# Kernel tuning notes

Hardware: AMD Instinct MI355X
Metric: run time of the kernel (lower is better)

## Reference

```python
import math
import jax, jax.numpy as jnp
import numpy as np

B, N, D, L = 8, 4096, 512, 64


def setup_inputs() -> dict:
    key = jax.random.key(0)
    ks = jax.random.split(key, 8)
    feats = jax.random.normal(ks[0], (B, N, D), dtype=jnp.float32)
    coords = jax.random.uniform(ks[1], (B, N, 2), dtype=jnp.float32)
    mask = jax.random.bernoulli(ks[2], 0.5, (B, N))  # True = padding (excluded)
    z = jax.random.normal(ks[3], (L, D), dtype=jnp.float32) * 0.02
    # xavier_uniform with gain=0.05 for square DxD weights: bound = gain*sqrt(6/(2D))
    bound = 0.05 * math.sqrt(6.0 / (2 * D))
    Wq = jax.random.uniform(ks[4], (D, D), minval=-bound, maxval=bound, dtype=jnp.float32)
    Wk = jax.random.uniform(ks[5], (D, D), minval=-bound, maxval=bound, dtype=jnp.float32)
    Wv = jax.random.uniform(ks[6], (D, D), minval=-bound, maxval=bound, dtype=jnp.float32)
    Wo = jax.random.uniform(ks[7], (D, D), minval=-bound, maxval=bound, dtype=jnp.float32)
    bo = jnp.zeros((D,), dtype=jnp.float32)
    return {"feats": feats, "coords": coords, "mask": mask, "z": z,
            "Wq": Wq, "Wk": Wk, "Wv": Wv, "Wo": Wo, "bo": bo}


def reference(feats, coords, mask, z, Wq, Wk, Wv, Wo, bo):
    Bb, Nn, Dd = feats.shape
    Ll = z.shape[0]
    temp = math.sqrt(Dd)
    q_all = z @ Wq.T  # [L, D] — one query per learned token

    def per_sample(f, m):
        nvalid = jnp.sum(~m)
        # stable sort: valid tokens (mask=False) first, original order preserved
        order = jnp.argsort(m.astype(jnp.int32), stable=True)
        sf = f[order]  # [N, D], first nvalid rows are the valid feats
        mu = sf.mean(-1, keepdims=True)
        var = sf.var(-1, keepdims=True)
        ln = (sf - mu) / jnp.sqrt(var + 1e-5)
        # segment assignment: seg_size = max(1, nvalid // L); token i -> segment i//seg_size
        seg_size = jnp.maximum(1, nvalid // Ll)
        pos = jnp.arange(Nn)
        seg = pos // seg_size
        tok_valid = (pos < nvalid) & (seg < Ll)  # tokens past L*seg_size are dropped (matches torch)
        seg_id = jnp.where(tok_valid, seg, Ll)  # dummy segment L for excluded tokens
        K = ln @ Wk.T  # [N, D]
        V = ln @ Wv.T  # [N, D]
        logits = jnp.clip(jnp.sum(q_all[jnp.minimum(seg, Ll - 1)] * K, -1) / temp, -5.0, 5.0)
        m_seg = jax.ops.segment_max(jnp.where(tok_valid, logits, -jnp.inf), seg_id, num_segments=Ll + 1)
        m_safe = jnp.where(jnp.isfinite(m_seg), m_seg, 0.0)
        e = jnp.where(tok_valid, jnp.exp(logits - m_safe[seg_id]), 0.0)
        denom = jax.ops.segment_sum(e, seg_id, num_segments=Ll + 1)[:Ll]            # [L]
        num = jax.ops.segment_sum(e[:, None] * V, seg_id, num_segments=Ll + 1)[:Ll]  # [L, D]
        nonempty = denom > 0
        Zattn = jnp.where(nonempty[:, None], num / jnp.maximum(denom, 1e-30)[:, None], z)
        out = Zattn @ Wo.T + bo
        return jnp.where(nvalid == 0, z, out)

    return jax.vmap(per_sample)(feats, mask)
```

## Files before the change

kernel.cpp:

```cpp
#include <hip/hip_runtime.h>
#include <math.h>

#define Bn 8
#define Nn 4096
#define Dn 512
#define Ln 64

template<int TN, bool BT, int NPART, bool SCALE>
__device__ __forceinline__ void gemm_tile(
    const float* __restrict__ A, size_t apstride, int m0,
    const float* __restrict__ B, int n0, int kbase, int ksteps,
    const float* __restrict__ sv,
    float* __restrict__ dst,
    float (*As)[68], float (*Bs)[132], int tid)
{
    const int ty = tid >> 4;
    const int tx = tid & 15;
    float acc[4][TN / 16];
    #pragma unroll
    for (int m = 0; m < 4; m++)
        #pragma unroll
        for (int n = 0; n < TN / 16; n++) acc[m][n] = 0.f;

    for (int s = 0; s < ksteps; s++) {
        const int k0 = kbase + s * 16;
        {
            int r = tid >> 2, kq = tid & 3;
            float4 v = *(const float4*)&A[(size_t)(m0 + r) * Dn + k0 + kq * 4];
            #pragma unroll
            for (int p = 1; p < NPART; p++) {
                float4 w = *(const float4*)&A[(size_t)p * apstride +
                                              (size_t)(m0 + r) * Dn + k0 + kq * 4];
                v.x += w.x; v.y += w.y; v.z += w.z; v.w += w.w;
            }
            if (SCALE) { float sc = sv[r]; v.x *= sc; v.y *= sc; v.z *= sc; v.w *= sc; }
            As[kq * 4 + 0][r] = v.x;
            As[kq * 4 + 1][r] = v.y;
            As[kq * 4 + 2][r] = v.z;
            As[kq * 4 + 3][r] = v.w;
        }
        #pragma unroll
        for (int rep = 0; rep < TN / 64; rep++) {
            int lin = tid + rep * 256;
            if (!BT) {
                int kk = lin / (TN / 4), jq = lin % (TN / 4);
                *(float4*)&Bs[kk][jq * 4] =
                    *(const float4*)&B[(size_t)(k0 + kk) * Dn + n0 + jq * 4];
            } else {
                int j = lin >> 2, kq = lin & 3;
                float4 v = *(const float4*)&B[(size_t)(n0 + j) * Dn + k0 + kq * 4];
                Bs[kq * 4 + 0][j] = v.x;
                Bs[kq * 4 + 1][j] = v.y;
                Bs[kq * 4 + 2][j] = v.z;
                Bs[kq * 4 + 3][j] = v.w;
            }
        }
        __syncthreads();
        #pragma unroll
        for (int kk = 0; kk < 16; kk++) {
            float4 a = *(const float4*)&As[kk][ty * 4];
            float av[4] = {a.x, a.y, a.z, a.w};
            if (TN == 64) {
                float4 b = *(const float4*)&Bs[kk][tx * 4];
                float bv[4] = {b.x, b.y, b.z, b.w};
                #pragma unroll
                for (int m = 0; m < 4; m++)
                    #pragma unroll
                    for (int n = 0; n < 4; n++) acc[m][n] += av[m] * bv[n];
            } else {
                float4 b0 = *(const float4*)&Bs[kk][tx * 8];
                float4 b1 = *(const float4*)&Bs[kk][tx * 8 + 4];
                float bv[8] = {b0.x, b0.y, b0.z, b0.w, b1.x, b1.y, b1.z, b1.w};
                #pragma unroll
                for (int m = 0; m < 4; m++)
                    #pragma unroll
                    for (int n = 0; n < 8; n++) acc[m][n % (TN/16)] += av[m] * bv[n];
            }
        }
        __syncthreads();
    }
    #pragma unroll
    for (int m = 0; m < 4; m++) {
        size_t base = (size_t)(m0 + ty * 4 + m) * Dn + n0;
        if (TN == 64) {
            float4 o = {acc[m][0], acc[m][1], acc[m][2], acc[m][3]};
            *(float4*)&dst[base + tx * 4] = o;
        } else {
            float4 o0 = {acc[m][0], acc[m][1], acc[m][2], acc[m][3]};
            float4 o1 = {acc[m][4], acc[m][5], acc[m][6], acc[m][7]};
            *(float4*)&dst[base + tx * 8] = o0;
            *(float4*)&dst[base + tx * 8 + 4] = o1;
        }
    }
}

__global__ void __launch_bounds__(256) kA_prep(
    const float* __restrict__ Wo, const float* __restrict__ Wv,
    const float* __restrict__ z,  const float* __restrict__ Wq,
    const unsigned char* __restrict__ maskbytes,
    float* __restrict__ wp, float* __restrict__ qp, float* __restrict__ wozp,
    int* __restrict__ nvalid, int* __restrict__ idx)
{
    __shared__ float As[16][68];
    __shared__ float Bs[16][132];
    __shared__ int scanbuf[256];
    __shared__ int cflags[4];

    int tid = threadIdx.x;
    int gb = blockIdx.x;

    if (gb < 256) {
        int ks = gb & 7;  int t = gb >> 3;
        int rt = t >> 2, ct = t & 3;
        gemm_tile<128, false, 1, false>(Wo, 0, rt * 64, Wv, ct * 128,
                                        ks * 64, 4, nullptr,
                                        wp + (size_t)ks * 262144, As, Bs, tid);
        return;
    }
    if (gb < 288) {
        int t = gb - 256; int ks = t & 3; int nt = t >> 2;
        gemm_tile<64, true, 1, false>(z, 0, 0, Wq, nt * 64,
                                      ks * 128, 8, nullptr,
                                      qp + (size_t)ks * 32768, As, Bs, tid);
        return;
    }
    if (gb < 320) {
        int t = gb - 288; int ks = t & 3; int nt = t >> 2;
        gemm_tile<64, true, 1, false>(z, 0, 0, Wo, nt * 64,
                                      ks * 128, 8, nullptr,
                                      wozp + (size_t)ks * 32768, As, Bs, tid);
        return;
    }

    int b = gb - 320;
    if (tid == 0) { cflags[0] = 0; cflags[1] = 0; cflags[2] = 0; }
    __syncthreads();
    int lge2 = 0, lb1 = 0, lm = 0;
    for (int p = tid; p < 4096; p += 256) {
        unsigned int v = maskbytes[p];
        if (v > 1u) lge2 = 1;
        if (v != 0u) {
            if ((p & 3) == 1) lb1 = 1;
            if ((p & 3) != 0) lm = 1;
        }
    }
    if (lge2) atomicOr(&cflags[0], 1);
    if (lb1)  atomicOr(&cflags[1], 1);
    if (lm)   atomicOr(&cflags[2], 1);
    __syncthreads();
    if (tid == 0) cflags[3] = cflags[0] ? (cflags[1] ? 2 : 4) : (cflags[2] ? 1 : 4);
    __syncthreads();
    int w = cflags[3];

    int base = tid * 16;
    int cnt = 0;
    int validbits[16];
    for (int e = 0; e < 16; e++) {
        int i = base + e;
        size_t byteoff = ((size_t)b * Nn + i) * (size_t)w;
        unsigned int nz = 0;
        for (int q = 0; q < w; q++) nz |= maskbytes[byteoff + q];
        int valid = (nz == 0) ? 1 : 0;
        validbits[e] = valid;
        cnt += valid;
    }
    scanbuf[tid] = cnt;
    __syncthreads();
    for (int off = 1; off < 256; off <<= 1) {
        int v = (tid >= off) ? scanbuf[tid - off] : 0;
        __syncthreads();
        scanbuf[tid] += v;
        __syncthreads();
    }
    int pos = scanbuf[tid] - cnt;
    for (int e = 0; e < 16; e++) {
        if (validbits[e]) { idx[b * Nn + pos] = base + e; pos++; }
    }
    if (tid == 255) nvalid[b] = scanbuf[255];
}

__global__ void __launch_bounds__(256) kB_qk(
    const float* __restrict__ qp, const float* __restrict__ Wk,
    const float* __restrict__ wp,
    float* __restrict__ qkp, float* __restrict__ wov)
{
    __shared__ float As[16][68];
    __shared__ float Bs[16][132];
    int tid = threadIdx.x;
    int gb = blockIdx.x;
    if (gb < 64) {
        int ks = gb & 7; int nt = gb >> 3;
        gemm_tile<64, false, 4, false>(qp, 32768, 0, Wk, nt * 64,
                                       ks * 64, 4, nullptr,
                                       qkp + (size_t)ks * 32768, As, Bs, tid);
        return;
    }
    int lin = (gb - 64) * 256 + tid;
    float4 v = {0.f, 0.f, 0.f, 0.f};
    #pragma unroll
    for (int p = 0; p < 8; p++) {
        float4 w = *(const float4*)&wp[(size_t)p * 262144 + (size_t)lin * 4];
        v.x += w.x; v.y += w.y; v.z += w.z; v.w += w.w;
    }
    *(float4*)&wov[(size_t)lin * 4] = v;
}

__global__ void __launch_bounds__(256) kE_tokens(
    const float* __restrict__ feats, const int* __restrict__ idx,
    const int* __restrict__ nvalid, const float* __restrict__ qkp,
    float* __restrict__ s_out, float* __restrict__ den_out)
{
    __shared__ float sred[4 * Dn];
    __shared__ float dred[4];
    int tid = threadIdx.x;
    int wv = tid >> 6;
    int lane = tid & 63;
    int b = blockIdx.x / Ln;
    int l = blockIdx.x % Ln;
    int nv = nvalid[b];
    int seg_size = nv / Ln; if (seg_size < 1) seg_size = 1;
    int used = Ln * seg_size; if (used > nv) used = nv;
    int r0 = l * seg_size;
    int r1 = r0 + seg_size; if (r1 > used) r1 = used;

    float4 qa = {0.f,0.f,0.f,0.f}, qb = {0.f,0.f,0.f,0.f};
    #pragma unroll
    for (int p = 0; p < 8; p++) {
        const float4* q4 = (const float4*)(qkp + (size_t)p * 32768 +
                                           (size_t)l * Dn + lane * 8);
        float4 a = q4[0], c = q4[1];
        qa.x += a.x; qa.y += a.y; qa.z += a.z; qa.w += a.w;
        qb.x += c.x; qb.y += c.y; qb.z += c.z; qb.w += c.w;
    }
    float qf[8] = {qa.x, qa.y, qa.z, qa.w, qb.x, qb.y, qb.z, qb.w};

    float sacc[8] = {0,0,0,0,0,0,0,0};
    float dacc = 0.f;
    const float inv_d = 1.0f / (float)Dn;
    const float inv_temp = 1.0f / 22.62741699796952f;

    for (int r = r0 + wv * 2; r < r1; r += 8) {
        int has2 = (r + 1 < r1);
        int t0 = idx[b * Nn + r];
        int t1 = has2 ? idx[b * Nn + r + 1] : t0;
        const float4* p0 = (const float4*)(feats + ((size_t)b * Nn + t0) * Dn + lane * 8);
        const float4* p1 = (const float4*)(feats + ((size_t)b * Nn + t1) * Dn + lane * 8);
        float4 xa0 = p0[0], xb0 = p0[1];
        float4 xa1 = p1[0], xb1 = p1[1];
        float x0[8] = {xa0.x, xa0.y, xa0.z, xa0.w, xb0.x, xb0.y, xb0.z, xb0.w};
        float x1[8] = {xa1.x, xa1.y, xa1.z, xa1.w, xb1.x, xb1.y, xb1.z, xb1.w};
        float sum0 = 0.f, ssq0 = 0.f, sum1 = 0.f, ssq1 = 0.f;
        #pragma unroll
        for (int j = 0; j < 8; j++) {
            sum0 += x0[j]; ssq0 += x0[j] * x0[j];
            sum1 += x1[j]; ssq1 += x1[j] * x1[j];
        }
        #pragma unroll
        for (int off = 32; off > 0; off >>= 1) {
            sum0 += __shfl_xor(sum0, off);
            ssq0 += __shfl_xor(ssq0, off);
            sum1 += __shfl_xor(sum1, off);
            ssq1 += __shfl_xor(ssq1, off);
        }
        float mu0 = sum0 * inv_d, mu1 = sum1 * inv_d;
        float rstd0 = rsqrtf(ssq0 * inv_d - mu0 * mu0 + 1e-5f);
        float rstd1 = rsqrtf(ssq1 * inv_d - mu1 * mu1 + 1e-5f);
        float ln0[8], ln1[8];
        float dot0 = 0.f, dot1 = 0.f;
        #pragma unroll
        for (int j = 0; j < 8; j++) {
            ln0[j] = (x0[j] - mu0) * rstd0; dot0 += ln0[j] * qf[j];
            ln1[j] = (x1[j] - mu1) * rstd1; dot1 += ln1[j] * qf[j];
        }
        #pragma unroll
        for (int off = 32; off > 0; off >>= 1) {
            dot0 += __shfl_xor(dot0, off);
            dot1 += __shfl_xor(dot1, off);
        }
        float lg0 = fminf(5.0f, fmaxf(-5.0f, dot0 * inv_temp));
        float lg1 = fminf(5.0f, fmaxf(-5.0f, dot1 * inv_temp));
        float e0 = expf(lg0);
        float e1 = has2 ? expf(lg1) : 0.f;
        #pragma unroll
        for (int j = 0; j < 8; j++) sacc[j] += e0 * ln0[j] + e1 * ln1[j];
        dacc += e0 + e1;
    }

    #pragma unroll
    for (int j = 0; j < 8; j++) sred[wv * Dn + lane * 8 + j] = sacc[j];
    if (lane == 0) dred[wv] = dacc;
    __syncthreads();
    for (int e = tid; e < Dn; e += 256) {
        float v = sred[e] + sred[Dn + e] + sred[2 * Dn + e] + sred[3 * Dn + e];
        s_out[(size_t)blockIdx.x * Dn + e] = v;
    }
    if (tid == 0) den_out[blockIdx.x] = dred[0] + dred[1] + dred[2] + dred[3];
}

__global__ void __launch_bounds__(256) kG_gemm(
    const float* __restrict__ s, const float* __restrict__ den,
    const float* __restrict__ wov, float* __restrict__ op)
{
    __shared__ float As[16][68];
    __shared__ float Bs[16][132];
    __shared__ float ssv[64];
    int tid = threadIdx.x;
    int gb = blockIdx.x;
    int ks = gb & 7; int t = gb >> 3;
    int rt = t >> 2, ct = t & 3;
    int m0 = rt * 64;
    if (tid < 64) {
        float dv = den[m0 + tid];
        ssv[tid] = (dv > 0.f) ? 1.f / dv : 0.f;
    }
    __syncthreads();
    gemm_tile<128, true, 1, true>(s, 0, m0, wov, ct * 128,
                                  ks * 64, 4, ssv,
                                  op + (size_t)ks * 262144, As, Bs, tid);
}

__global__ void __launch_bounds__(256) kH_epilogue(
    const float* __restrict__ op, const float* __restrict__ den,
    const int* __restrict__ nvalid, const float* __restrict__ wozp,
    const float* __restrict__ z, const float* __restrict__ bo,
    float* __restrict__ out)
{
    int lin = blockIdx.x * 256 + threadIdx.x;
    int row = lin >> 7;
    int col = (lin & 127) * 4;
    int b = row >> 6, l = row & 63;
    float4 v;
    if (nvalid[b] == 0) {
        v = *(const float4*)&z[(size_t)l * Dn + col];
    } else {
        float4 bv = *(const float4*)&bo[col];
        float dv = den[row];
        if (dv > 0.f) {
            float4 a = {0.f, 0.f, 0.f, 0.f};
            #pragma unroll
            for (int p = 0; p < 8; p++) {
                float4 w = *(const float4*)&op[(size_t)p * 262144 + (size_t)row * Dn + col];
                a.x += w.x; a.y += w.y; a.z += w.z; a.w += w.w;
            }
            v.x = a.x + bv.x; v.y = a.y + bv.y; v.z = a.z + bv.z; v.w = a.w + bv.w;
        } else {
            float4 a = {0.f, 0.f, 0.f, 0.f};
            #pragma unroll
            for (int p = 0; p < 4; p++) {
                float4 w = *(const float4*)&wozp[(size_t)p * 32768 + (size_t)l * Dn + col];
                a.x += w.x; a.y += w.y; a.z += w.z; a.w += w.w;
            }
            v.x = a.x + bv.x; v.y = a.y + bv.y; v.z = a.z + bv.z; v.w = a.w + bv.w;
        }
    }
    *(float4*)&out[(size_t)row * Dn + col] = v;
}

extern "C" void kernel_launch(void* const* d_in, const int* in_sizes, int n_in,
                              void* d_out, int out_size, void* d_ws, size_t ws_size,
                              hipStream_t stream) {
    const float* feats = (const float*)d_in[0];
    const unsigned char* maskb = (const unsigned char*)d_in[2];
    const float* z  = (const float*)d_in[3];
    const float* Wq = (const float*)d_in[4];
    const float* Wk = (const float*)d_in[5];
    const float* Wv = (const float*)d_in[6];
    const float* Wo = (const float*)d_in[7];
    const float* bo = (const float*)d_in[8];
    float* out = (float*)d_out;

    int*   nvalid = (int*)d_ws;
    int*   idx    = nvalid + 64;
    float* fbase  = (float*)(idx + Bn * Nn);
    float* qp     = fbase;
    float* wozp   = qp   + 4 * 32768;
    float* qkp    = wozp + 4 * 32768;
    float* wov    = qkp  + 8 * 32768;
    float* sbuf   = wov  + 262144;
    float* den    = sbuf + 262144;
    float* wp     = den  + 1024;
    float* op     = wp;

    kA_prep<<<328, 256, 0, stream>>>(Wo, Wv, z, Wq, maskb, wp, qp, wozp, nvalid, idx);
    kB_qk<<<320, 256, 0, stream>>>(qp, Wk, wp, qkp, wov);
    kE_tokens<<<Bn * Ln, 256, 0, stream>>>(feats, idx, nvalid, qkp, sbuf, den);
    kG_gemm<<<256, 256, 0, stream>>>(sbuf, den, wov, op);
    kH_epilogue<<<256, 256, 0, stream>>>(op, den, nvalid, wozp, z, bo, out);
}
```

Baseline: 148.9 us.

## Fuse five kernels into one cooperative kernel with grid-wide syncs

Merges the prep, QK/Wov reduction, token, GEMM and epilogue kernels into a single cooperative launch of 512 blocks, with grid.sync() between phases. The aim is to remove four kernel launch boundaries and their drain and ramp gaps. In exchange every phase runs on a fixed 512-block grid, so some phases leave blocks idle. Shared memory per block rises to the union of all phases, and grid syncs add their own cost. Residency of 512 blocks must be guaranteed for the cooperative launch to succeed.

```diff
diff --git a/kernel.cpp b/kernel.cpp
--- a/kernel.cpp
+++ b/kernel.cpp
@@ -1,5 +1,8 @@
 #include <hip/hip_runtime.h>
+#include <hip/hip_cooperative_groups.h>
 #include <math.h>
+
+namespace cg = cooperative_groups;
 
 #define Bn 8
 #define Nn 4096
@@ -8,10 +11,10 @@
 
 template<int TN, bool BT, int NPART, bool SCALE>
 __device__ __forceinline__ void gemm_tile(
-    const float* __restrict__ A, size_t apstride, int m0,
-    const float* __restrict__ B, int n0, int kbase, int ksteps,
-    const float* __restrict__ sv,
-    float* __restrict__ dst,
+    const float* A, size_t apstride, int m0,
+    const float* B, int n0, int kbase, int ksteps,
+    const float* sv,
+    float* dst,
     float (*As)[68], float (*Bs)[132], int tid)
 {
     const int ty = tid >> 4;
@@ -94,17 +97,24 @@
     }
 }
 
-__global__ void __launch_bounds__(256) kA_prep(
-    const float* __restrict__ Wo, const float* __restrict__ Wv,
-    const float* __restrict__ z,  const float* __restrict__ Wq,
-    const unsigned char* __restrict__ maskbytes,
-    float* __restrict__ wp, float* __restrict__ qp, float* __restrict__ wozp,
-    int* __restrict__ nvalid, int* __restrict__ idx)
+__global__ void __launch_bounds__(256) k_fused(
+    const float* __restrict__ feats, const unsigned char* __restrict__ maskbytes,
+    const float* __restrict__ z, const float* __restrict__ Wq,
+    const float* __restrict__ Wk, const float* __restrict__ Wv,
+    const float* __restrict__ Wo, const float* __restrict__ bo,
+    float* __restrict__ out,
+    int* nvalid, int* idx, float* qp, float* wozp, float* qkp,
+    float* wov, float* sbuf, float* den, float* wp)
 {
+    cg::grid_group grid = cg::this_grid();
+
     __shared__ float As[16][68];
     __shared__ float Bs[16][132];
     __shared__ int scanbuf[256];
     __shared__ int cflags[4];
+    __shared__ float sred[4 * Dn];
+    __shared__ float dred[4];
+    __shared__ float ssv[64];
 
     int tid = threadIdx.x;
     int gb = blockIdx.x;
@@ -115,245 +125,219 @@
         gemm_tile<128, false, 1, false>(Wo, 0, rt * 64, Wv, ct * 128,
                                         ks * 64, 4, nullptr,
                                         wp + (size_t)ks * 262144, As, Bs, tid);
-        return;
-    }
-    if (gb < 288) {
+    } else if (gb < 288) {
         int t = gb - 256; int ks = t & 3; int nt = t >> 2;
         gemm_tile<64, true, 1, false>(z, 0, 0, Wq, nt * 64,
                                       ks * 128, 8, nullptr,
                                       qp + (size_t)ks * 32768, As, Bs, tid);
-        return;
-    }
-    if (gb < 320) {
+    } else if (gb < 320) {
         int t = gb - 288; int ks = t & 3; int nt = t >> 2;
         gemm_tile<64, true, 1, false>(z, 0, 0, Wo, nt * 64,
                                       ks * 128, 8, nullptr,
                                       wozp + (size_t)ks * 32768, As, Bs, tid);
-        return;
-    }
-
-    int b = gb - 320;
-    if (tid == 0) { cflags[0] = 0; cflags[1] = 0; cflags[2] = 0; }
-    __syncthreads();
-    int lge2 = 0, lb1 = 0, lm = 0;
-    for (int p = tid; p < 4096; p += 256) {
-        unsigned int v = maskbytes[p];
-        if (v > 1u) lge2 = 1;
-        if (v != 0u) {
-            if ((p & 3) == 1) lb1 = 1;
-            if ((p & 3) != 0) lm = 1;
-        }
-    }
-    if (lge2) atomicOr(&cflags[0], 1);
-    if (lb1)  atomicOr(&cflags[1], 1);
-    if (lm)   atomicOr(&cflags[2], 1);
-    __syncthreads();
-    if (tid == 0) cflags[3] = cflags[0] ? (cflags[1] ? 2 : 4) : (cflags[2] ? 1 : 4);
-    __syncthreads();
-    int w = cflags[3];
-
-    int base = tid * 16;
-    int cnt = 0;
-    int validbits[16];
-    for (int e = 0; e < 16; e++) {
-        int i = base + e;
-        size_t byteoff = ((size_t)b * Nn + i) * (size_t)w;
-        unsigned int nz = 0;
-        for (int q = 0; q < w; q++) nz |= maskbytes[byteoff + q];
-        int valid = (nz == 0) ? 1 : 0;
-        validbits[e] = valid;
-        cnt += valid;
-    }
-    scanbuf[tid] = cnt;
-    __syncthreads();
-    for (int off = 1; off < 256; off <<= 1) {
-        int v = (tid >= off) ? scanbuf[tid - off] : 0;
-        __syncthreads();
-        scanbuf[tid] += v;
-        __syncthreads();
-    }
-    int pos = scanbuf[tid] - cnt;
-    for (int e = 0; e < 16; e++) {
-        if (validbits[e]) { idx[b * Nn + pos] = base + e; pos++; }
-    }
-    if (tid == 255) nvalid[b] = scanbuf[255];
-}
-
-__global__ void __launch_bounds__(256) kB_qk(
-    const float* __restrict__ qp, const float* __restrict__ Wk,
-    const float* __restrict__ wp,
-    float* __restrict__ qkp, float* __restrict__ wov)
-{
-    __shared__ float As[16][68];
-    __shared__ float Bs[16][132];
-    int tid = threadIdx.x;
-    int gb = blockIdx.x;
+    } else if (gb < 328) {
+        int b = gb - 320;
+        if (tid == 0) { cflags[0] = 0; cflags[1] = 0; cflags[2] = 0; }
+        __syncthreads();
+        int lge2 = 0, lb1 = 0, lm = 0;
+        for (int p = tid; p < 4096; p += 256) {
+            unsigned int v = maskbytes[p];
+            if (v > 1u) lge2 = 1;
+            if (v != 0u) {
+                if ((p & 3) == 1) lb1 = 1;
+                if ((p & 3) != 0) lm = 1;
+            }
+        }
+        if (lge2) atomicOr(&cflags[0], 1);
+        if (lb1)  atomicOr(&cflags[1], 1);
+        if (lm)   atomicOr(&cflags[2], 1);
+        __syncthreads();
+        if (tid == 0) cflags[3] = cflags[0] ? (cflags[1] ? 2 : 4) : (cflags[2] ? 1 : 4);
+        __syncthreads();
+        int w = cflags[3];
+
+        int base = tid * 16;
+        int cnt = 0;
+        int validbits[16];
+        for (int e = 0; e < 16; e++) {
+            int i = base + e;
+            size_t byteoff = ((size_t)b * Nn + i) * (size_t)w;
+            unsigned int nz = 0;
+            for (int q = 0; q < w; q++) nz |= maskbytes[byteoff + q];
+            int valid = (nz == 0) ? 1 : 0;
+            validbits[e] = valid;
+            cnt += valid;
+        }
+        scanbuf[tid] = cnt;
+        __syncthreads();
+        for (int off = 1; off < 256; off <<= 1) {
+            int v = (tid >= off) ? scanbuf[tid - off] : 0;
+            __syncthreads();
+            scanbuf[tid] += v;
+            __syncthreads();
+        }
+        int pos = scanbuf[tid] - cnt;
+        for (int e = 0; e < 16; e++) {
+            if (validbits[e]) { idx[b * Nn + pos] = base + e; pos++; }
+        }
+        if (tid == 255) nvalid[b] = scanbuf[255];
+    }
+    __threadfence();
+    grid.sync();
+
     if (gb < 64) {
         int ks = gb & 7; int nt = gb >> 3;
         gemm_tile<64, false, 4, false>(qp, 32768, 0, Wk, nt * 64,
                                        ks * 64, 4, nullptr,
                                        qkp + (size_t)ks * 32768, As, Bs, tid);
-        return;
-    }
-    int lin = (gb - 64) * 256 + tid;
-    float4 v = {0.f, 0.f, 0.f, 0.f};
-    #pragma unroll
-    for (int p = 0; p < 8; p++) {
-        float4 w = *(const float4*)&wp[(size_t)p * 262144 + (size_t)lin * 4];
-        v.x += w.x; v.y += w.y; v.z += w.z; v.w += w.w;
-    }
-    *(float4*)&wov[(size_t)lin * 4] = v;
-}
-
-__global__ void __launch_bounds__(256) kE_tokens(
-    const float* __restrict__ feats, const int* __restrict__ idx,
-    const int* __restrict__ nvalid, const float* __restrict__ qkp,
-    float* __restrict__ s_out, float* __restrict__ den_out)
-{
-    __shared__ float sred[4 * Dn];
-    __shared__ float dred[4];
-    int tid = threadIdx.x;
-    int wv = tid >> 6;
-    int lane = tid & 63;
-    int b = blockIdx.x / Ln;
-    int l = blockIdx.x % Ln;
-    int nv = nvalid[b];
-    int seg_size = nv / Ln; if (seg_size < 1) seg_size = 1;
-    int used = Ln * seg_size; if (used > nv) used = nv;
-    int r0 = l * seg_size;
-    int r1 = r0 + seg_size; if (r1 > used) r1 = used;
-
-    float4 qa = {0.f,0.f,0.f,0.f}, qb = {0.f,0.f,0.f,0.f};
-    #pragma unroll
-    for (int p = 0; p < 8; p++) {
-        const float4* q4 = (const float4*)(qkp + (size_t)p * 32768 +
-                                           (size_t)l * Dn + lane * 8);
-        float4 a = q4[0], c = q4[1];
-        qa.x += a.x; qa.y += a.y; qa.z += a.z; qa.w += a.w;
-        qb.x += c.x; qb.y += c.y; qb.z += c.z; qb.w += c.w;
-    }
-    float qf[8] = {qa.x, qa.y, qa.z, qa.w, qb.x, qb.y, qb.z, qb.w};
-
-    float sacc[8] = {0,0,0,0,0,0,0,0};
-    float dacc = 0.f;
-    const float inv_d = 1.0f / (float)Dn;
-    const float inv_temp = 1.0f / 22.62741699796952f;
-
-    for (int r = r0 + wv * 2; r < r1; r += 8) {
-        int has2 = (r + 1 < r1);
-        int t0 = idx[b * Nn + r];
-        int t1 = has2 ? idx[b * Nn + r + 1] : t0;
-        const float4* p0 = (const float4*)(feats + ((size_t)b * Nn + t0) * Dn + lane * 8);
-        const float4* p1 = (const float4*)(feats + ((size_t)b * Nn + t1) * Dn + lane * 8);
-        float4 xa0 = p0[0], xb0 = p0[1];
-        float4 xa1 = p1[0], xb1 = p1[1];
-        float x0[8] = {xa0.x, xa0.y, xa0.z, xa0.w, xb0.x, xb0.y, xb0.z, xb0.w};
-        float x1[8] = {xa1.x, xa1.y, xa1.z, xa1.w, xb1.x, xb1.y, xb1.z, xb1.w};
-        float sum0 = 0.f, ssq0 = 0.f, sum1 = 0.f, ssq1 = 0.f;
-        #pragma unroll
-        for (int j = 0; j < 8; j++) {
-            sum0 += x0[j]; ssq0 += x0[j] * x0[j];
-            sum1 += x1[j]; ssq1 += x1[j] * x1[j];
-        }
-        #pragma unroll
-        for (int off = 32; off > 0; off >>= 1) {
-            sum0 += __shfl_xor(sum0, off);
-            ssq0 += __shfl_xor(ssq0, off);
-            sum1 += __shfl_xor(sum1, off);
-            ssq1 += __shfl_xor(ssq1, off);
-        }
-        float mu0 = sum0 * inv_d, mu1 = sum1 * inv_d;
-        float rstd0 = rsqrtf(ssq0 * inv_d - mu0 * mu0 + 1e-5f);
-        float rstd1 = rsqrtf(ssq1 * inv_d - mu1 * mu1 + 1e-5f);
-        float ln0[8], ln1[8];
-        float dot0 = 0.f, dot1 = 0.f;
-        #pragma unroll
-        for (int j = 0; j < 8; j++) {
-            ln0[j] = (x0[j] - mu0) * rstd0; dot0 += ln0[j] * qf[j];
-            ln1[j] = (x1[j] - mu1) * rstd1; dot1 += ln1[j] * qf[j];
-        }
-        #pragma unroll
-        for (int off = 32; off > 0; off >>= 1) {
-            dot0 += __shfl_xor(dot0, off);
-            dot1 += __shfl_xor(dot1, off);
-        }
-        float lg0 = fminf(5.0f, fmaxf(-5.0f, dot0 * inv_temp));
-        float lg1 = fminf(5.0f, fmaxf(-5.0f, dot1 * inv_temp));
-        float e0 = expf(lg0);
-        float e1 = has2 ? expf(lg1) : 0.f;
-        #pragma unroll
-        for (int j = 0; j < 8; j++) sacc[j] += e0 * ln0[j] + e1 * ln1[j];
-        dacc += e0 + e1;
-    }
-
-    #pragma unroll
-    for (int j = 0; j < 8; j++) sred[wv * Dn + lane * 8 + j] = sacc[j];
-    if (lane == 0) dred[wv] = dacc;
-    __syncthreads();
-    for (int e = tid; e < Dn; e += 256) {
-        float v = sred[e] + sred[Dn + e] + sred[2 * Dn + e] + sred[3 * Dn + e];
-        s_out[(size_t)blockIdx.x * Dn + e] = v;
-    }
-    if (tid == 0) den_out[blockIdx.x] = dred[0] + dred[1] + dred[2] + dred[3];
-}
-
-__global__ void __launch_bounds__(256) kG_gemm(
-    const float* __restrict__ s, const float* __restrict__ den,
-    const float* __restrict__ wov, float* __restrict__ op)
-{
-    __shared__ float As[16][68];
-    __shared__ float Bs[16][132];
-    __shared__ float ssv[64];
-    int tid = threadIdx.x;
-    int gb = blockIdx.x;
-    int ks = gb & 7; int t = gb >> 3;
-    int rt = t >> 2, ct = t & 3;
-    int m0 = rt * 64;
-    if (tid < 64) {
-        float dv = den[m0 + tid];
-        ssv[tid] = (dv > 0.f) ? 1.f / dv : 0.f;
-    }
-    __syncthreads();
-    gemm_tile<128, true, 1, true>(s, 0, m0, wov, ct * 128,
-                                  ks * 64, 4, ssv,
-                                  op + (size_t)ks * 262144, As, Bs, tid);
-}
-
-__global__ void __launch_bounds__(256) kH_epilogue(
-    const float* __restrict__ op, const float* __restrict__ den,
-    const int* __restrict__ nvalid, const float* __restrict__ wozp,
-    const float* __restrict__ z, const float* __restrict__ bo,
-    float* __restrict__ out)
-{
-    int lin = blockIdx.x * 256 + threadIdx.x;
-    int row = lin >> 7;
-    int col = (lin & 127) * 4;
-    int b = row >> 6, l = row & 63;
-    float4 v;
-    if (nvalid[b] == 0) {
-        v = *(const float4*)&z[(size_t)l * Dn + col];
-    } else {
-        float4 bv = *(const float4*)&bo[col];
-        float dv = den[row];
-        if (dv > 0.f) {
-            float4 a = {0.f, 0.f, 0.f, 0.f};
-            #pragma unroll
-            for (int p = 0; p < 8; p++) {
-                float4 w = *(const float4*)&op[(size_t)p * 262144 + (size_t)row * Dn + col];
-                a.x += w.x; a.y += w.y; a.z += w.z; a.w += w.w;
-            }
-            v.x = a.x + bv.x; v.y = a.y + bv.y; v.z = a.z + bv.z; v.w = a.w + bv.w;
+    } else if (gb < 320) {
+        int lin = (gb - 64) * 256 + tid;
+        float4 v = {0.f, 0.f, 0.f, 0.f};
+        #pragma unroll
+        for (int p = 0; p < 8; p++) {
+            float4 w = *(const float4*)&wp[(size_t)p * 262144 + (size_t)lin * 4];
+            v.x += w.x; v.y += w.y; v.z += w.z; v.w += w.w;
+        }
+        *(float4*)&wov[(size_t)lin * 4] = v;
+    }
+    __threadfence();
+    grid.sync();
+
+    {
+        int wv = tid >> 6;
+        int lane = tid & 63;
+        int b = gb / Ln;
+        int l = gb % Ln;
+        int nv = nvalid[b];
+        int seg_size = nv / Ln; if (seg_size < 1) seg_size = 1;
+        int used = Ln * seg_size; if (used > nv) used = nv;
+        int r0 = l * seg_size;
+        int r1 = r0 + seg_size; if (r1 > used) r1 = used;
+
+        float4 qa = {0.f,0.f,0.f,0.f}, qb = {0.f,0.f,0.f,0.f};
+        #pragma unroll
+        for (int p = 0; p < 8; p++) {
+            const float4* q4 = (const float4*)(qkp + (size_t)p * 32768 +
+                                               (size_t)l * Dn + lane * 8);
+            float4 a = q4[0], c = q4[1];
+            qa.x += a.x; qa.y += a.y; qa.z += a.z; qa.w += a.w;
+            qb.x += c.x; qb.y += c.y; qb.z += c.z; qb.w += c.w;
+        }
+        float qf[8] = {qa.x, qa.y, qa.z, qa.w, qb.x, qb.y, qb.z, qb.w};
+
+        float sacc[8] = {0,0,0,0,0,0,0,0};
+        float dacc = 0.f;
+        const float inv_d = 1.0f / (float)Dn;
+        const float inv_temp = 1.0f / 22.62741699796952f;
+
+        for (int r = r0 + wv * 2; r < r1; r += 8) {
+            int has2 = (r + 1 < r1);
+            int t0 = idx[b * Nn + r];
+            int t1 = has2 ? idx[b * Nn + r + 1] : t0;
+            const float4* p0 = (const float4*)(feats + ((size_t)b * Nn + t0) * Dn + lane * 8);
+            const float4* p1 = (const float4*)(feats + ((size_t)b * Nn + t1) * Dn + lane * 8);
+            float4 xa0 = p0[0], xb0 = p0[1];
+            float4 xa1 = p1[0], xb1 = p1[1];
+            float x0[8] = {xa0.x, xa0.y, xa0.z, xa0.w, xb0.x, xb0.y, xb0.z, xb0.w};
+            float x1[8] = {xa1.x, xa1.y, xa1.z, xa1.w, xb1.x, xb1.y, xb1.z, xb1.w};
+            float sum0 = 0.f, ssq0 = 0.f, sum1 = 0.f, ssq1 = 0.f;
+            #pragma unroll
+            for (int j = 0; j < 8; j++) {
+                sum0 += x0[j]; ssq0 += x0[j] * x0[j];
+                sum1 += x1[j]; ssq1 += x1[j] * x1[j];
+            }
+            #pragma unroll
+            for (int off = 32; off > 0; off >>= 1) {
+                sum0 += __shfl_xor(sum0, off);
+                ssq0 += __shfl_xor(ssq0, off);
+                sum1 += __shfl_xor(sum1, off);
+                ssq1 += __shfl_xor(ssq1, off);
+            }
+            float mu0 = sum0 * inv_d, mu1 = sum1 * inv_d;
+            float rstd0 = rsqrtf(ssq0 * inv_d - mu0 * mu0 + 1e-5f);
+            float rstd1 = rsqrtf(ssq1 * inv_d - mu1 * mu1 + 1e-5f);
+            float ln0[8], ln1[8];
+            float dot0 = 0.f, dot1 = 0.f;
+            #pragma unroll
+            for (int j = 0; j < 8; j++) {
+                ln0[j] = (x0[j] - mu0) * rstd0; dot0 += ln0[j] * qf[j];
+                ln1[j] = (x1[j] - mu1) * rstd1; dot1 += ln1[j] * qf[j];
+            }
+            #pragma unroll
+            for (int off = 32; off > 0; off >>= 1) {
+                dot0 += __shfl_xor(dot0, off);
+                dot1 += __shfl_xor(dot1, off);
+            }
+            float lg0 = fminf(5.0f, fmaxf(-5.0f, dot0 * inv_temp));
+            float lg1 = fminf(5.0f, fmaxf(-5.0f, dot1 * inv_temp));
+            float e0 = expf(lg0);
+            float e1 = has2 ? expf(lg1) : 0.f;
+            #pragma unroll
+            for (int j = 0; j < 8; j++) sacc[j] += e0 * ln0[j] + e1 * ln1[j];
+            dacc += e0 + e1;
+        }
+
+        #pragma unroll
+        for (int j = 0; j < 8; j++) sred[wv * Dn + lane * 8 + j] = sacc[j];
+        if (lane == 0) dred[wv] = dacc;
+        __syncthreads();
+        for (int e = tid; e < Dn; e += 256) {
+            float v = sred[e] + sred[Dn + e] + sred[2 * Dn + e] + sred[3 * Dn + e];
+            sbuf[(size_t)gb * Dn + e] = v;
+        }
+        if (tid == 0) den[gb] = dred[0] + dred[1] + dred[2] + dred[3];
+    }
+    __threadfence();
+    grid.sync();
+
+    if (gb < 256) {
+        int ks = gb & 7; int t = gb >> 3;
+        int rt = t >> 2, ct = t & 3;
+        int m0 = rt * 64;
+        if (tid < 64) {
+            float dv = den[m0 + tid];
+            ssv[tid] = (dv > 0.f) ? 1.f / dv : 0.f;
+        }
+        __syncthreads();
+        gemm_tile<128, true, 1, true>(sbuf, 0, m0, wov, ct * 128,
+                                      ks * 64, 4, ssv,
+                                      wp + (size_t)ks * 262144, As, Bs, tid);
+    }
+    __threadfence();
+    grid.sync();
+
+    if (gb < 256) {
+        const float* op = wp;
+        int lin = gb * 256 + tid;
+        int row = lin >> 7;
+        int col = (lin & 127) * 4;
+        int b = row >> 6, l = row & 63;
+        float4 v;
+        if (nvalid[b] == 0) {
+            v = *(const float4*)&z[(size_t)l * Dn + col];
         } else {
-            float4 a = {0.f, 0.f, 0.f, 0.f};
-            #pragma unroll
-            for (int p = 0; p < 4; p++) {
-                float4 w = *(const float4*)&wozp[(size_t)p * 32768 + (size_t)l * Dn + col];
-                a.x += w.x; a.y += w.y; a.z += w.z; a.w += w.w;
-            }
-            v.x = a.x + bv.x; v.y = a.y + bv.y; v.z = a.z + bv.z; v.w = a.w + bv.w;
-        }
-    }
-    *(float4*)&out[(size_t)row * Dn + col] = v;
+            float4 bv = *(const float4*)&bo[col];
+            float dv = den[row];
+            if (dv > 0.f) {
+                float4 a = {0.f, 0.f, 0.f, 0.f};
+                #pragma unroll
+                for (int p = 0; p < 8; p++) {
+                    float4 w = *(const float4*)&op[(size_t)p * 262144 + (size_t)row * Dn + col];
+                    a.x += w.x; a.y += w.y; a.z += w.z; a.w += w.w;
+                }
+                v.x = a.x + bv.x; v.y = a.y + bv.y; v.z = a.z + bv.z; v.w = a.w + bv.w;
+            } else {
+                float4 a = {0.f, 0.f, 0.f, 0.f};
+                #pragma unroll
+                for (int p = 0; p < 4; p++) {
+                    float4 w = *(const float4*)&wozp[(size_t)p * 32768 + (size_t)l * Dn + col];
+                    a.x += w.x; a.y += w.y; a.z += w.z; a.w += w.w;
+                }
+                v.x = a.x + bv.x; v.y = a.y + bv.y; v.z = a.z + bv.z; v.w = a.w + bv.w;
+            }
+        }
+        *(float4*)&out[(size_t)row * Dn + col] = v;
+    }
 }
 
 extern "C" void kernel_launch(void* const* d_in, const int* in_sizes, int n_in,
@@ -379,11 +363,13 @@
     float* sbuf   = wov  + 262144;
     float* den    = sbuf + 262144;
     float* wp     = den  + 1024;
-    float* op     = wp;
-
-    kA_prep<<<328, 256, 0, stream>>>(Wo, Wv, z, Wq, maskb, wp, qp, wozp, nvalid, idx);
-    kB_qk<<<320, 256, 0, stream>>>(qp, Wk, wp, qkp, wov);
-    kE_tokens<<<Bn * Ln, 256, 0, stream>>>(feats, idx, nvalid, qkp, sbuf, den);
-    kG_gemm<<<256, 256, 0, stream>>>(sbuf, den, wov, op);
-    kH_epilogue<<<256, 256, 0, stream>>>(op, den, nvalid, wozp, z, bo, out);
+
+    void* kargs[] = {
+        (void*)&feats, (void*)&maskb, (void*)&z, (void*)&Wq, (void*)&Wk,
+        (void*)&Wv, (void*)&Wo, (void*)&bo, (void*)&out,
+        (void*)&nvalid, (void*)&idx, (void*)&qp, (void*)&wozp, (void*)&qkp,
+        (void*)&wov, (void*)&sbuf, (void*)&den, (void*)&wp
+    };
+    hipLaunchCooperativeKernel((const void*)k_fused, dim3(512), dim3(256),
+                               kargs, 0, stream);
 }
```

Result: slower. 582.8 us (+291.4%).
